# Performance work log

Measured on AMD Instinct MI355X. Metric: run time of the kernel, lower is better.

Reference implementation:

```python
import jax, jax.numpy as jnp
import numpy as np

BINS = 30
MOMENTUM = 0.75
LOSS_WEIGHT = 1.0


def setup_inputs() -> dict:
    key = jax.random.key(0)
    k1, k2 = jax.random.split(key)
    B, C = 16384, 1000
    preds = jax.random.normal(k1, (B, C), dtype=jnp.float32)
    targets = jax.random.randint(k2, (B, C), 0, 2).astype(jnp.float32)
    acc_sum = jnp.zeros((BINS,), dtype=jnp.float32)
    return {"preds": preds, "targets": targets, "acc_sum": acc_sum}


def reference(preds, targets, acc_sum):
    # gradient magnitude g = |sigmoid(p) - t|, detached in the original
    g = jax.lax.stop_gradient(jnp.abs(jax.nn.sigmoid(preds) - targets))
    tot = jnp.float32(preds.size)

    # bin index: edges are i/BINS with last edge bumped by 1e-6, so g==1 -> last bin
    bin_idx = jnp.minimum((g * BINS).astype(jnp.int32), BINS - 1)

    # single-pass histogram (replaces the per-bin masked reductions)
    counts = jnp.zeros((BINS,), dtype=jnp.float32).at[bin_idx.ravel()].add(1.0)
    nonzero = counts > 0

    # momentum-updated accumulator only where the bin is populated
    new_acc = jnp.where(nonzero, MOMENTUM * acc_sum + (1.0 - MOMENTUM) * counts, acc_sum)
    per_bin_w = jnp.where(nonzero, tot / jnp.where(nonzero, new_acc, 1.0), 0.0)

    n = jnp.sum(nonzero.astype(jnp.float32))
    n = jnp.maximum(n, 1.0)

    # gather per-element weights, normalize by number of populated bins
    weights = jax.lax.stop_gradient(per_bin_w[bin_idx] / n)

    # stable BCE-with-logits, weighted, mean reduction
    x, t = preds, targets
    bce = jnp.maximum(x, 0.0) - x * t + jnp.log1p(jnp.exp(-jnp.abs(x)))
    loss = jnp.mean(weights * bce)
    return loss * LOSS_WEIGHT
```

## Files before the change

### kernel.cpp

```cpp
#include <hip/hip_runtime.h>

#define BINS 30
#define BLOCK 256
#define GRID 512
#define GSTRIDE 32

__device__ __forceinline__ float fast_exp2(float x){ return __builtin_amdgcn_exp2f(x); }
__device__ __forceinline__ float fast_log2(float x){ return __builtin_amdgcn_logf(x); }
__device__ __forceinline__ float fast_rcp (float x){ return __builtin_amdgcn_rcpf(x); }

#define LOG2E 1.4426950408889634f
#define LN2   0.6931471805599453f

__global__ __launch_bounds__(BLOCK) void ghm_pass1(
    const float4* __restrict__ preds4, const float4* __restrict__ targets4,
    long n4, long n_total,
    float* __restrict__ gCnt, float* __restrict__ gSum)
{
    __shared__ float2 hist[BINS][BLOCK];

    const int tid = threadIdx.x;
    #pragma unroll
    for (int b = 0; b < BINS; ++b) hist[b][tid] = make_float2(0.0f, 0.0f);
    __syncthreads();

    auto do4 = [&](float4 p, float4 t) {
        #pragma unroll
        for (int j = 0; j < 4; ++j) {
            float x  = (&p.x)[j];
            float tt = (&t.x)[j];
            float y  = __builtin_fmaf(x * tt, -2.0f, x);
            float e  = fast_exp2(fabsf(y) * -LOG2E);
            float d  = 1.0f + e;
            float r  = fast_rcp(d);
            float g  = (y >= 0.0f) ? r : e * r;
            int   b  = (int)(g * 30.0f);
            b = (b > BINS - 1) ? BINS - 1 : b;
            float bce = fmaxf(y, 0.0f) + fast_log2(d) * LN2;
            float2 h = hist[b][tid];
            h.x += 1.0f;
            h.y += bce;
            hist[b][tid] = h;
        }
    };

    const long stride = (long)gridDim.x * BLOCK;
    long i = (long)blockIdx.x * BLOCK + tid;
    for (; i + stride < n4; i += 2 * stride) {
        float4 p0 = preds4[i];
        float4 t0 = targets4[i];
        float4 p1 = preds4[i + stride];
        float4 t1 = targets4[i + stride];
        do4(p0, t0);
        do4(p1, t1);
    }
    for (; i < n4; i += stride) {
        do4(preds4[i], targets4[i]);
    }

    long tail0 = n4 * 4;
    if (blockIdx.x == 0 && tail0 + tid < n_total) {
        float x  = ((const float*)preds4)[tail0 + tid];
        float tt = ((const float*)targets4)[tail0 + tid];
        float y  = __builtin_fmaf(x * tt, -2.0f, x);
        float e  = fast_exp2(fabsf(y) * -LOG2E);
        float d  = 1.0f + e;
        float r  = fast_rcp(d);
        float g  = (y >= 0.0f) ? r : e * r;
        int   b  = (int)(g * 30.0f);
        b = (b > BINS - 1) ? BINS - 1 : b;
        float bce = fmaxf(y, 0.0f) + fast_log2(d) * LN2;
        float2 h = hist[b][tid];
        h.x += 1.0f; h.y += bce;
        hist[b][tid] = h;
    }
    __syncthreads();

    for (int k = 7; k >= 0; --k) {
        int s = 1 << k;
        for (int i2 = tid; i2 < (BINS << k); i2 += BLOCK) {
            int b = i2 >> k;
            int c = i2 & (s - 1);
            float2 a  = hist[b][c];
            float2 d2 = hist[b][c + s];
            hist[b][c] = make_float2(a.x + d2.x, a.y + d2.y);
        }
        __syncthreads();
    }

    if (tid < BINS) {
        float2 h = hist[tid][0];
        if (h.x != 0.0f) {
            atomicAdd(&gCnt[tid * GSTRIDE], h.x);
            atomicAdd(&gSum[tid * GSTRIDE], h.y);
        }
    }
}

__global__ void ghm_final(const float* __restrict__ gCnt,
                          const float* __restrict__ gSum,
                          const float* __restrict__ acc_sum,
                          float* __restrict__ out)
{
    int b = threadIdx.x;
    float val = 0.0f, nz = 0.0f;
    if (b < BINS) {
        float c = gCnt[b * GSTRIDE];
        if (c > 0.0f) {
            float na = 0.75f * acc_sum[b] + 0.25f * c;
            val = gSum[b * GSTRIDE] / na;
            nz  = 1.0f;
        }
    }
    #pragma unroll
    for (int m = 32; m >= 1; m >>= 1) {
        val += __shfl_xor(val, m);
        nz  += __shfl_xor(nz,  m);
    }
    if (b == 0) out[0] = val / fmaxf(nz, 1.0f);
}

extern "C" void kernel_launch(void* const* d_in, const int* in_sizes, int n_in,
                              void* d_out, int out_size, void* d_ws, size_t ws_size,
                              hipStream_t stream)
{
    const float* preds   = (const float*)d_in[0];
    const float* targets = (const float*)d_in[1];
    const float* acc_sum = (const float*)d_in[2];

    float* gCnt = (float*)d_ws;
    float* gSum = gCnt + BINS * GSTRIDE;

    long n  = (long)in_sizes[0];
    long n4 = n / 4;

    hipMemsetAsync(d_ws, 0, 2 * BINS * GSTRIDE * sizeof(float), stream);

    long want = (n4 + BLOCK - 1) / BLOCK;
    int blocks = (int)((want < GRID) ? (want > 1 ? want : 1) : GRID);

    ghm_pass1<<<blocks, BLOCK, 0, stream>>>((const float4*)preds,
                                            (const float4*)targets,
                                            n4, n, gCnt, gSum);
    ghm_final<<<1, 64, 0, stream>>>(gCnt, gSum, acc_sum, (float*)d_out);
}
```

Before: 36.64 us.

## Replace LDS histogram with register cumulative step-function counters in packed fp16

```diff
diff --git a/kernel.cpp b/kernel.cpp
--- a/kernel.cpp
+++ b/kernel.cpp
@@ -2,12 +2,14 @@
 
 #define BINS 30
 #define BLOCK 256
-#define GRID 512
+#define GRID 768
 #define GSTRIDE 32
+#define KSTEP 4096.0f
+
+typedef __fp16 f16x2 __attribute__((ext_vector_type(2)));
 
 __device__ __forceinline__ float fast_exp2(float x){ return __builtin_amdgcn_exp2f(x); }
 __device__ __forceinline__ float fast_log2(float x){ return __builtin_amdgcn_logf(x); }
-__device__ __forceinline__ float fast_rcp (float x){ return __builtin_amdgcn_rcpf(x); }
 
 #define LOG2E 1.4426950408889634f
 #define LN2   0.6931471805599453f
@@ -17,83 +19,82 @@
     long n4, long n_total,
     float* __restrict__ gCnt, float* __restrict__ gSum)
 {
-    __shared__ float2 hist[BINS][BLOCK];
+    const float nthr[30] = {
+        8.192e29f,
+        KSTEP*3.3673323f,  KSTEP*2.6390573f,  KSTEP*2.1972246f,  KSTEP*1.8718022f,
+        KSTEP*1.6094379f,  KSTEP*1.3862944f,  KSTEP*1.1895841f,  KSTEP*1.0116009f,
+        KSTEP*0.8472979f,  KSTEP*0.6931472f,  KSTEP*0.5465437f,  KSTEP*0.4054651f,
+        KSTEP*0.2682640f,  KSTEP*0.1335314f,  0.0f,
+        -KSTEP*0.1335314f, -KSTEP*0.2682640f, -KSTEP*0.4054651f, -KSTEP*0.5465437f,
+        -KSTEP*0.6931472f, -KSTEP*0.8472979f, -KSTEP*1.0116009f, -KSTEP*1.1895841f,
+        -KSTEP*1.3862944f, -KSTEP*1.6094379f, -KSTEP*1.8718022f, -KSTEP*2.1972246f,
+        -KSTEP*2.6390573f, -KSTEP*3.3673323f };
+
+    f16x2 cnt[15], sum[15];
+    #pragma unroll
+    for (int p = 0; p < 15; ++p) {
+        cnt[p] = (f16x2){(__fp16)0.0f, (__fp16)0.0f};
+        sum[p] = (f16x2){(__fp16)0.0f, (__fp16)0.0f};
+    }
 
     const int tid = threadIdx.x;
-    #pragma unroll
-    for (int b = 0; b < BINS; ++b) hist[b][tid] = make_float2(0.0f, 0.0f);
-    __syncthreads();
 
-    auto do4 = [&](float4 p, float4 t) {
+    auto proc = [&](float x, float tt) {
+        float y   = __builtin_fmaf(x * tt, -2.0f, x);
+        float yk  = y * KSTEP;
+        float e   = fast_exp2(fabsf(y) * -LOG2E);
+        float bce = fmaxf(y, 0.0f) + fast_log2(1.0f + e) * LN2;
+        f16x2 bce2 = __builtin_amdgcn_cvt_pkrtz(bce, bce);
         #pragma unroll
-        for (int j = 0; j < 4; ++j) {
-            float x  = (&p.x)[j];
-            float tt = (&t.x)[j];
-            float y  = __builtin_fmaf(x * tt, -2.0f, x);
-            float e  = fast_exp2(fabsf(y) * -LOG2E);
-            float d  = 1.0f + e;
-            float r  = fast_rcp(d);
-            float g  = (y >= 0.0f) ? r : e * r;
-            int   b  = (int)(g * 30.0f);
-            b = (b > BINS - 1) ? BINS - 1 : b;
-            float bce = fmaxf(y, 0.0f) + fast_log2(d) * LN2;
-            float2 h = hist[b][tid];
-            h.x += 1.0f;
-            h.y += bce;
-            hist[b][tid] = h;
+        for (int p = 0; p < 15; ++p) {
+            float s0, s1;
+            asm("v_add_f32 %0, %1, %2 clamp" : "=v"(s0) : "s"(nthr[2*p]),   "v"(yk));
+            asm("v_add_f32 %0, %1, %2 clamp" : "=v"(s1) : "s"(nthr[2*p+1]), "v"(yk));
+            f16x2 s2 = __builtin_amdgcn_cvt_pkrtz(s0, s1);
+            cnt[p] += s2;
+            sum[p] += s2 * bce2;
         }
     };
 
     const long stride = (long)gridDim.x * BLOCK;
-    long i = (long)blockIdx.x * BLOCK + tid;
-    for (; i + stride < n4; i += 2 * stride) {
-        float4 p0 = preds4[i];
-        float4 t0 = targets4[i];
-        float4 p1 = preds4[i + stride];
-        float4 t1 = targets4[i + stride];
-        do4(p0, t0);
-        do4(p1, t1);
-    }
-    for (; i < n4; i += stride) {
-        do4(preds4[i], targets4[i]);
+    for (long i = (long)blockIdx.x * BLOCK + tid; i < n4; i += stride) {
+        float4 p = preds4[i];
+        float4 t = targets4[i];
+        #pragma unroll
+        for (int j = 0; j < 4; ++j) proc((&p.x)[j], (&t.x)[j]);
     }
 
     long tail0 = n4 * 4;
     if (blockIdx.x == 0 && tail0 + tid < n_total) {
-        float x  = ((const float*)preds4)[tail0 + tid];
-        float tt = ((const float*)targets4)[tail0 + tid];
-        float y  = __builtin_fmaf(x * tt, -2.0f, x);
-        float e  = fast_exp2(fabsf(y) * -LOG2E);
-        float d  = 1.0f + e;
-        float r  = fast_rcp(d);
-        float g  = (y >= 0.0f) ? r : e * r;
-        int   b  = (int)(g * 30.0f);
-        b = (b > BINS - 1) ? BINS - 1 : b;
-        float bce = fmaxf(y, 0.0f) + fast_log2(d) * LN2;
-        float2 h = hist[b][tid];
-        h.x += 1.0f; h.y += bce;
-        hist[b][tid] = h;
+        proc(((const float*)preds4)[tail0 + tid],
+             ((const float*)targets4)[tail0 + tid]);
+    }
+
+    __shared__ float sC[4][BINS];
+    __shared__ float sS[4][BINS];
+    const int lane = tid & 63, wave = tid >> 6;
+
+    #pragma unroll
+    for (int p = 0; p < 15; ++p) {
+        float c0 = (float)cnt[p][0], c1 = (float)cnt[p][1];
+        float s0 = (float)sum[p][0], s1 = (float)sum[p][1];
+        #pragma unroll
+        for (int m = 32; m >= 1; m >>= 1) {
+            c0 += __shfl_xor(c0, m);  c1 += __shfl_xor(c1, m);
+            s0 += __shfl_xor(s0, m);  s1 += __shfl_xor(s1, m);
+        }
+        if (lane == 0) {
+            sC[wave][2*p] = c0;  sC[wave][2*p+1] = c1;
+            sS[wave][2*p] = s0;  sS[wave][2*p+1] = s1;
+        }
     }
     __syncthreads();
 
-    for (int k = 7; k >= 0; --k) {
-        int s = 1 << k;
-        for (int i2 = tid; i2 < (BINS << k); i2 += BLOCK) {
-            int b = i2 >> k;
-            int c = i2 & (s - 1);
-            float2 a  = hist[b][c];
-            float2 d2 = hist[b][c + s];
-            hist[b][c] = make_float2(a.x + d2.x, a.y + d2.y);
-        }
-        __syncthreads();
-    }
-
     if (tid < BINS) {
-        float2 h = hist[tid][0];
-        if (h.x != 0.0f) {
-            atomicAdd(&gCnt[tid * GSTRIDE], h.x);
-            atomicAdd(&gSum[tid * GSTRIDE], h.y);
-        }
+        float c = sC[0][tid] + sC[1][tid] + sC[2][tid] + sC[3][tid];
+        float s = sS[0][tid] + sS[1][tid] + sS[2][tid] + sS[3][tid];
+        atomicAdd(&gCnt[tid * GSTRIDE], c);
+        atomicAdd(&gSum[tid * GSTRIDE], s);
     }
 }
 
@@ -105,10 +106,13 @@
     int b = threadIdx.x;
     float val = 0.0f, nz = 0.0f;
     if (b < BINS) {
-        float c = gCnt[b * GSTRIDE];
-        if (c > 0.0f) {
-            float na = 0.75f * acc_sum[b] + 0.25f * c;
-            val = gSum[b * GSTRIDE] / na;
+        float Cb  = gCnt[b * GSTRIDE];
+        float Cb1 = (b < 29) ? gCnt[(b + 1) * GSTRIDE] : 0.0f;
+        float cb  = Cb - Cb1;
+        if (cb > 0.5f) {
+            float Sb = gSum[b * GSTRIDE] - ((b < 29) ? gSum[(b + 1) * GSTRIDE] : 0.0f);
+            float na = 0.75f * acc_sum[b] + 0.25f * cb;
+            val = Sb / na;
             nz  = 1.0f;
         }
     }
```

Result: slower. 63.63 us (+73.7%).
